# Optimization experiments

Hardware: AMD Instinct MI355X
Metric: run time of the kernel (lower is better)

## Reference

```python
import jax, jax.numpy as jnp
import numpy as np

HEADS = 1
EPS = 1e-12  # torch F.normalize eps


def dwt_haar(x):
    # Haar analysis, J=1, zero mode (even H,W -> no padding needed).
    b, c, H, W = x.shape
    xr = x.reshape(b, c, H // 2, 2, W // 2, 2)
    a = xr[:, :, :, 0, :, 0]
    bb = xr[:, :, :, 0, :, 1]
    cc = xr[:, :, :, 1, :, 0]
    d = xr[:, :, :, 1, :, 1]
    ll = (a + bb + cc + d) * 0.5
    h1 = (a - bb + cc - d) * 0.5  # high in width
    h2 = (a + bb - cc - d) * 0.5  # high in height
    h3 = (a - bb - cc + d) * 0.5  # diagonal
    return ll, h1, h2, h3


def idwt_haar(ll, h1, h2, h3):
    a = (ll + h1 + h2 + h3) * 0.5
    bb = (ll - h1 + h2 - h3) * 0.5
    cc = (ll + h1 - h2 - h3) * 0.5
    d = (ll - h1 - h2 + h3) * 0.5
    row0 = jnp.stack([a, bb], axis=-1)   # (b,c,h2,w2,2)
    row1 = jnp.stack([cc, d], axis=-1)
    y = jnp.stack([row0, row1], axis=3)  # (b,c,h2,2,w2,2)
    b_, c_, h2_, _, w2_, _ = y.shape
    return y.reshape(b_, c_, h2_ * 2, w2_ * 2)


def conv1x1(x, w, bias):
    # x: (b,c,h,w); w: (o,c); bias: (o,)
    return jnp.einsum('oc,bchw->bohw', w, x) + bias[None, :, None, None]


def mdta(x, qw, qb, kw, kb, vw, vb, pw, pb, temp):
    b, c, h, w = x.shape
    q = conv1x1(x, qw, qb).reshape(b, HEADS, c // HEADS, h * w)
    k = conv1x1(x, kw, kb).reshape(b, HEADS, c // HEADS, h * w)
    v = conv1x1(x, vw, vb).reshape(b, HEADS, c // HEADS, h * w)
    q = q / jnp.maximum(jnp.linalg.norm(q, axis=-1, keepdims=True), EPS)
    k = k / jnp.maximum(jnp.linalg.norm(k, axis=-1, keepdims=True), EPS)
    attn = jnp.einsum('bhcn,bhdn->bhcd', q, k) * temp[None]
    attn = jax.nn.softmax(attn, axis=-1)
    out = jnp.einsum('bhcd,bhdn->bhcn', attn, v).reshape(b, c, h, w)
    return conv1x1(out, pw, pb)


def setup_inputs() -> dict:
    key = jax.random.key(0)
    ks = jax.random.split(key, 20)
    B, C, H, W = 16, 64, 256, 256
    C3 = 3 * C
    s1 = 1.0 / np.sqrt(C)
    s3 = 1.0 / np.sqrt(C3)
    d = {'img': jax.random.normal(ks[0], (B, C, H, W), jnp.float32)}
    names = ['qw', 'qb', 'kw', 'kb', 'vw', 'vb', 'pw', 'pb']
    for i, n in enumerate(names):
        if n.endswith('w'):
            d['ll_' + n] = jax.random.normal(ks[1 + i], (C, C), jnp.float32) * s1
            d['h_' + n] = jax.random.normal(ks[10 + i], (C3, C3), jnp.float32) * s3
        else:
            d['ll_' + n] = jax.random.normal(ks[1 + i], (C,), jnp.float32) * s1
            d['h_' + n] = jax.random.normal(ks[10 + i], (C3,), jnp.float32) * s3
    d['ll_temp'] = jnp.ones((HEADS, 1, 1), jnp.float32)
    d['h_temp'] = jnp.ones((HEADS, 1, 1), jnp.float32)
    return d


def reference(img, ll_qw, ll_qb, ll_kw, ll_kb, ll_vw, ll_vb, ll_pw, ll_pb, ll_temp,
              h_qw, h_qb, h_kw, h_kb, h_vw, h_vb, h_pw, h_pb, h_temp):
    b, c, H, W = img.shape
    ll, h1, h2, h3 = dwt_haar(img)
    # rearrange 'b c fp h w -> b (c fp) h w' with fp=3 (bands interleaved per channel)
    hh = jnp.stack([h1, h2, h3], axis=2).reshape(b, c * 3, H // 2, W // 2)
    ll = mdta(ll, ll_qw, ll_qb, ll_kw, ll_kb, ll_vw, ll_vb, ll_pw, ll_pb, ll_temp)
    hh = mdta(hh, h_qw, h_qb, h_kw, h_kb, h_vw, h_vb, h_pw, h_pb, h_temp)
    hh = hh.reshape(b, c, 3, H // 2, W // 2)
    return idwt_haar(ll, hh[:, :, 0], hh[:, :, 1], hh[:, :, 2])
```

## Files before the change

### kernel.cpp

```cpp
#include <hip/hip_runtime.h>

typedef __bf16 bf16;
typedef bf16 bf16x8 __attribute__((ext_vector_type(8)));
typedef bf16 bf16x4 __attribute__((ext_vector_type(4)));
typedef float f32x4 __attribute__((ext_vector_type(4)));

#define NB 16
#define CLL 64
#define CHH 192
#define NPIX 16384

__global__ __launch_bounds__(256) void k_dwt(const float* __restrict__ img, bf16* __restrict__ xll,
                      bf16* __restrict__ xhh, float* __restrict__ sll, float* __restrict__ shh) {
    int bc = blockIdx.y;
    int b = bc >> 6, c = bc & 63;
    int t = threadIdx.x;
    int r = blockIdx.x * 16 + (t >> 4);
    int q = t & 15;
    const float* p0 = img + ((size_t)bc << 16) + (size_t)(2 * r) * 256 + 16 * q;
    const float* p1 = p0 + 256;
    float4 e0[4], e1[4];
    #pragma unroll
    for (int l = 0; l < 4; l++) { e0[l] = ((const float4*)p0)[l]; e1[l] = ((const float4*)p1)[l]; }
    const float* f0 = (const float*)e0;
    const float* f1 = (const float*)e1;
    bf16x8 vll, v1, v2, v3;
    float s0 = 0.f, s1 = 0.f, s2 = 0.f, s3 = 0.f;
    #pragma unroll
    for (int p = 0; p < 8; p++) {
        float a = f0[2 * p], bb = f0[2 * p + 1], cc = f1[2 * p], d = f1[2 * p + 1];
        float wll = (a + bb + cc + d) * 0.5f;
        float w1  = (a - bb + cc - d) * 0.5f;
        float w2  = (a + bb - cc - d) * 0.5f;
        float w3  = (a - bb - cc + d) * 0.5f;
        vll[p] = (bf16)wll; v1[p] = (bf16)w1; v2[p] = (bf16)w2; v3[p] = (bf16)w3;
        s0 += wll; s1 += w1; s2 += w2; s3 += w3;
    }
    size_t n = (size_t)r * 128 + 8 * q;
    *(bf16x8*)(xll + ((size_t)b * CLL + c) * NPIX + n) = vll;
    size_t hb = ((size_t)b * CHH + 3 * c) * NPIX + n;
    *(bf16x8*)(xhh + hb) = v1;
    *(bf16x8*)(xhh + hb + NPIX) = v2;
    *(bf16x8*)(xhh + hb + 2 * NPIX) = v3;
    for (int o = 32; o; o >>= 1) {
        s0 += __shfl_down(s0, o); s1 += __shfl_down(s1, o);
        s2 += __shfl_down(s2, o); s3 += __shfl_down(s3, o);
    }
    if ((t & 63) == 0) {
        atomicAdd(&sll[b * CLL + c], s0);
        atomicAdd(&shh[b * CHH + 3 * c + 0], s1);
        atomicAdd(&shh[b * CHH + 3 * c + 1], s2);
        atomicAdd(&shh[b * CHH + 3 * c + 2], s3);
    }
}

template <int C, int SPLITK>
__global__ __launch_bounds__(256) void k_gram(const bf16* __restrict__ X, float* __restrict__ G) {
    constexpr int T = C / 64;
    constexpr int NT = T * (T + 1) / 2;
    constexpr int KC = NPIX / SPLITK;
    __shared__ bf16 sA[64 * 64];
    __shared__ bf16 sB[64 * 64];
    int id = blockIdx.x;
    int sk = id % SPLITK; id /= SPLITK;
    int tl = id % NT;     id /= NT;
    int b = id;
    int ti = 0, tt = tl;
    while (tt >= T - ti) { tt -= T - ti; ti++; }
    int tj = ti + tt;
    const bf16* Xb = X + (size_t)b * C * NPIX;
    int t = threadIdx.x;
    int lane = t & 63, wv = t >> 6;
    int g = lane >> 4, l15 = lane & 15;

    int rowi = t >> 3, chunk = t & 7;
    int k0 = sk * KC;
    const bf16* gA0 = Xb + (size_t)(ti * 64 + rowi) * NPIX + k0 + chunk * 8;
    const bf16* gA1 = gA0 + (size_t)32 * NPIX;
    const bf16* gB0 = Xb + (size_t)(tj * 64 + rowi) * NPIX + k0 + chunk * 8;
    const bf16* gB1 = gB0 + (size_t)32 * NPIX;
    int swc = (chunk ^ (rowi & 7)) * 8;
    bf16* lA0 = sA + rowi * 64 + swc;
    bf16* lA1 = sA + (rowi + 32) * 64 + swc;
    bf16* lB0 = sB + rowi * 64 + swc;
    bf16* lB1 = sB + (rowi + 32) * 64 + swc;

    int arow = (wv >> 1) * 32;
    int bcol = (wv & 1) * 32;
    int sw = l15 & 7;
    int roA0 = (arow + l15) * 64, roA1 = roA0 + 16 * 64;
    int roB0 = (bcol + l15) * 64, roB1 = roB0 + 16 * 64;

    f32x4 acc[2][2] = {};
    bf16x8 rA0 = *(const bf16x8*)gA0;
    bf16x8 rA1 = *(const bf16x8*)gA1;
    bf16x8 rB0 = *(const bf16x8*)gB0;
    bf16x8 rB1 = *(const bf16x8*)gB1;
    for (int kc = 0; kc < KC; kc += 64) {
        *(bf16x8*)lA0 = rA0; *(bf16x8*)lA1 = rA1;
        *(bf16x8*)lB0 = rB0; *(bf16x8*)lB1 = rB1;
        __syncthreads();
        if (kc + 64 < KC) {
            rA0 = *(const bf16x8*)(gA0 + kc + 64);
            rA1 = *(const bf16x8*)(gA1 + kc + 64);
            rB0 = *(const bf16x8*)(gB0 + kc + 64);
            rB1 = *(const bf16x8*)(gB1 + kc + 64);
        }
        #pragma unroll
        for (int ks = 0; ks < 2; ks++) {
            int ck = ((ks * 4 + g) ^ sw) * 8;
            bf16x8 a0 = *(const bf16x8*)(sA + roA0 + ck);
            bf16x8 a1 = *(const bf16x8*)(sA + roA1 + ck);
            bf16x8 b0 = *(const bf16x8*)(sB + roB0 + ck);
            bf16x8 b1 = *(const bf16x8*)(sB + roB1 + ck);
            acc[0][0] = __builtin_amdgcn_mfma_f32_16x16x32_bf16(a0, b0, acc[0][0], 0, 0, 0);
            acc[0][1] = __builtin_amdgcn_mfma_f32_16x16x32_bf16(a0, b1, acc[0][1], 0, 0, 0);
            acc[1][0] = __builtin_amdgcn_mfma_f32_16x16x32_bf16(a1, b0, acc[1][0], 0, 0, 0);
            acc[1][1] = __builtin_amdgcn_mfma_f32_16x16x32_bf16(a1, b1, acc[1][1], 0, 0, 0);
        }
        __syncthreads();
    }
    float* Gb = G + (size_t)b * C * C;
    int r0q = ti * 64 + arow;
    int c0q = tj * 64 + bcol;
    #pragma unroll
    for (int rr = 0; rr < 2; rr++)
        #pragma unroll
        for (int c2 = 0; c2 < 2; c2++)
            #pragma unroll
            for (int rg = 0; rg < 4; rg++) {
                int row = r0q + rr * 16 + g * 4 + rg;
                int col = c0q + c2 * 16 + l15;
                atomicAdd(&Gb[(size_t)row * C + col], acc[rr][c2][rg]);
            }
}

__global__ void k_prep(float* __restrict__ Gll, float* __restrict__ Ghh,
                       const float* __restrict__ llvw, const float* __restrict__ hvw,
                       float* __restrict__ vwTll, float* __restrict__ vwThh) {
    const int S1 = CLL * CLL, S2 = CLL * CLL + CHH * CHH;
    int b = blockIdx.y;
    int idx = blockIdx.x * 256 + threadIdx.x;
    if (idx < S1) {
        float* Gb = Gll + (size_t)b * S1;
        int i = idx / CLL, j = idx % CLL;
        if (j < i) Gb[idx] = Gb[(size_t)j * CLL + i];
    } else if (idx < S2) {
        int id2 = idx - S1;
        float* Gb = Ghh + (size_t)b * (CHH * CHH);
        int i = id2 / CHH, j = id2 % CHH;
        if (j < i) Gb[id2] = Gb[(size_t)j * CHH + i];
    } else if (b == 0) {
        int k2 = idx - S2;
        if (k2 < S1) {
            int r = k2 / CLL, k = k2 % CLL;
            vwTll[k2] = llvw[(size_t)k * CLL + r];
        } else {
            int k3 = k2 - S1;
            if (k3 < CHH * CHH) {
                int r = k3 / CHH, k = k3 % CHH;
                vwThh[k3] = hvw[(size_t)k * CHH + r];
            }
        }
    }
}

template <typename OUT>
__global__ __launch_bounds__(256) void k_ntu(
        const float* __restrict__ Xll0, const float* __restrict__ Xll1, long XllbS,
        const float* __restrict__ Yll, long YllbS,
        OUT* __restrict__ Oll, long OllzS, long OllbS,
        const float* __restrict__ Xhh0, const float* __restrict__ Xhh1, long XhhbS,
        const float* __restrict__ Yhh, long YhhbS,
        OUT* __restrict__ Ohh, long OhhzS, long OhhbS) {
    int x = blockIdx.x, b = blockIdx.y, z = blockIdx.z;
    int C, rt, ct;
    const float *X, *Y;
    OUT* O;
    if (x == 0) {
        C = CLL; rt = 0; ct = 0;
        X = (z ? Xll1 : Xll0) + (size_t)b * XllbS;
        Y = Yll + (size_t)b * YllbS;
        O = Oll + (size_t)z * OllzS + (size_t)b * OllbS;
    } else {
        C = CHH; int tl = x - 1; rt = tl / 3; ct = tl % 3;
        X = (z ? Xhh1 : Xhh0) + (size_t)b * XhhbS;
        Y = Yhh + (size_t)b * YhhbS;
        O = Ohh + (size_t)z * OhhzS + (size_t)b * OhhbS;
    }
    int t = threadIdx.x, ti = t >> 4, tj = t & 15;
    const float* xr = X + (size_t)(rt * 64 + ti * 4) * C;
    const float* yr = Y + (size_t)(ct * 64 + tj * 4) * C;
    float acc[4][4] = {};
    for (int k = 0; k < C; k += 4) {
        float4 xa[4], yb[4];
        #pragma unroll
        for (int a = 0; a < 4; a++) xa[a] = *(const float4*)(xr + (size_t)a * C + k);
        #pragma unroll
        for (int q = 0; q < 4; q++) yb[q] = *(const float4*)(yr + (size_t)q * C + k);
        #pragma unroll
        for (int a = 0; a < 4; a++)
            #pragma unroll
            for (int q = 0; q < 4; q++)
                acc[a][q] += xa[a].x * yb[q].x + xa[a].y * yb[q].y
                           + xa[a].z * yb[q].z + xa[a].w * yb[q].w;
    }
    #pragma unroll
    for (int a = 0; a < 4; a++) {
        int row = rt * 64 + ti * 4 + a, col = ct * 64 + tj * 4;
        if constexpr (sizeof(OUT) == 4) {
            *(float4*)((float*)O + (size_t)row * C + col) =
                make_float4(acc[a][0], acc[a][1], acc[a][2], acc[a][3]);
        } else {
            bf16x4 v;
            v[0] = (bf16)acc[a][0]; v[1] = (bf16)acc[a][1];
            v[2] = (bf16)acc[a][2]; v[3] = (bf16)acc[a][3];
            *(bf16x4*)((bf16*)O + (size_t)row * C + col) = v;
        }
    }
}

__global__ __launch_bounds__(256) void k_nrm(const float* __restrict__ PRll,
        const float* __restrict__ PRhh,
        const float* __restrict__ llqw, const float* __restrict__ llkw,
        const float* __restrict__ hqw,  const float* __restrict__ hkw,
        const float* __restrict__ llqb, const float* __restrict__ llkb,
        const float* __restrict__ hqb,  const float* __restrict__ hkb,
        const float* __restrict__ sll,  const float* __restrict__ shh,
        float* __restrict__ nrmll, float* __restrict__ nrmhh,
        float* __restrict__ wsll,  float* __restrict__ wshh) {
    int z = blockIdx.z, b = blockIdx.y;
    int wv = threadIdx.x >> 6, lane = threadIdx.x & 63;
    int gr = blockIdx.x * 4 + wv;
    int C, i; const float *P, *w, *wb, *s; float *nrm, *ws;
    if (gr < CLL) {
        C = CLL; i = gr;
        P = PRll + ((size_t)z * NB + b) * CLL * CLL;
        w = z ? llkw : llqw; wb = z ? llkb : llqb;
        s = sll + (size_t)b * CLL;
        nrm = nrmll + ((size_t)z * NB + b) * CLL;
        ws  = wsll  + ((size_t)z * NB + b) * CLL;
    } else {
        C = CHH; i = gr - CLL;
        P = PRhh + ((size_t)z * NB + b) * CHH * CHH;
        w = z ? hkw : hqw; wb = z ? hkb : hqb;
        s = shh + (size_t)b * CHH;
        nrm = nrmhh + ((size_t)z * NB + b) * CHH;
        ws  = wshh  + ((size_t)z * NB + b) * CHH;
    }
    const float* Pi = P + (size_t)i * C;
    const float* wi = w + (size_t)i * C;
    float np = 0.f, sd = 0.f;
    for (int j = lane; j < C; j += 64) {
        float wj = wi[j];
        np += Pi[j] * wj;
        sd += wj * s[j];
    }
    for (int o = 32; o; o >>= 1) { np += __shfl_down(np, o); sd += __shfl_down(sd, o); }
    if (lane == 0) {
        float wbi = wb[i];
        float q2 = np + 2.f * wbi * sd + (float)NPIX * wbi * wbi;
        nrm[i] = fmaxf(sqrtf(fmaxf(q2, 0.f)), 1e-12f);
        ws[i] = sd;
    }
}

__global__ __launch_bounds__(256) void k_soft2(
        const float* __restrict__ Lll, const float* __restrict__ Lhh,
        const float* __restrict__ llkb, const float* __restrict__ llqb,
        const float* __restrict__ hkb,  const float* __restrict__ hqb,
        const float* __restrict__ nrmll, const float* __restrict__ nrmhh,
        const float* __restrict__ wsll,  const float* __restrict__ wshh,
        const float* __restrict__ llvb,  const float* __restrict__ hvb,
        const float* __restrict__ lltp,  const float* __restrict__ htp,
        float* __restrict__ All, float* __restrict__ Ahh,
        float* __restrict__ avll, float* __restrict__ avhh) {
    int b = blockIdx.y;
    int wv = threadIdx.x >> 6, lane = threadIdx.x & 63;
    int gr = blockIdx.x * 4 + wv;
    int C, i; const float *Lb, *kb, *qb, *qn, *kn, *qs, *ks, *vb, *tp;
    float *A, *av;
    if (gr < CLL) {
        C = CLL; i = gr;
        Lb = Lll + (size_t)b * CLL * CLL; kb = llkb; qb = llqb;
        qn = nrmll + (size_t)b * CLL;  kn = nrmll + ((size_t)NB + b) * CLL;
        qs = wsll + (size_t)b * CLL;   ks = wsll + ((size_t)NB + b) * CLL;
        vb = llvb; tp = lltp;
        A = All + (size_t)b * CLL * CLL; av = avll + (size_t)b * CLL;
    } else {
        C = CHH; i = gr - CLL;
        Lb = Lhh + (size_t)b * CHH * CHH; kb = hkb; qb = hqb;
        qn = nrmhh + (size_t)b * CHH;  kn = nrmhh + ((size_t)NB + b) * CHH;
        qs = wshh + (size_t)b * CHH;   ks = wshh + ((size_t)NB + b) * CHH;
        vb = hvb; tp = htp;
        A = Ahh + (size_t)b * CHH * CHH; av = avhh + (size_t)b * CHH;
    }
    const float* Li = Lb + (size_t)i * C;
    float qni = qn[i], qsi = qs[i], qbi = qb[i], tmp = tp[0];
    float Lv[3];
    #pragma unroll
    for (int s2 = 0; s2 < 3; s2++) {
        int j = lane + s2 * 64;
        if (j < C) {
            float l = Li[j] + qsi * kb[j] + qbi * ks[j] + (float)NPIX * qbi * kb[j];
            Lv[s2] = l / (qni * kn[j]) * tmp;
        } else Lv[s2] = -1e30f;
    }
    float mx = fmaxf(fmaxf(Lv[0], Lv[1]), Lv[2]);
    for (int o = 32; o; o >>= 1) mx = fmaxf(mx, __shfl_xor(mx, o));
    float e[3], sum = 0.f;
    #pragma unroll
    for (int s2 = 0; s2 < 3; s2++) {
        e[s2] = (lane + s2 * 64 < C) ? expf(Lv[s2] - mx) : 0.f;
        sum += e[s2];
    }
    for (int o = 32; o; o >>= 1) sum += __shfl_xor(sum, o);
    float inv = 1.f / sum;
    float avp = 0.f;
    #pragma unroll
    for (int s2 = 0; s2 < 3; s2++) {
        int j = lane + s2 * 64;
        if (j < C) {
            float a = e[s2] * inv;
            A[(size_t)i * C + j] = a;
            avp += a * vb[j];
        }
    }
    for (int o = 32; o; o >>= 1) avp += __shfl_down(avp, o);
    if (lane == 0) av[i] = avp;
}

__global__ __launch_bounds__(256) void k_mv(const float* __restrict__ llpw,
        const float* __restrict__ llpb, const float* __restrict__ hpw,
        const float* __restrict__ hpb, const float* __restrict__ avll,
        const float* __restrict__ avhh, float* __restrict__ mvll, float* __restrict__ mvhh) {
    int b = blockIdx.y;
    int wv = threadIdx.x >> 6, lane = threadIdx.x & 63;
    int gr = blockIdx.x * 4 + wv;
    int C, i; const float *pw, *pb_, *av_; float* mv_;
    if (gr < CLL) {
        C = CLL; i = gr;
        pw = llpw; pb_ = llpb; av_ = avll + (size_t)b * CLL; mv_ = mvll + (size_t)b * CLL;
    } else {
        C = CHH; i = gr - CLL;
        pw = hpw; pb_ = hpb; av_ = avhh + (size_t)b * CHH; mv_ = mvhh + (size_t)b * CHH;
    }
    const float* pwi = pw + (size_t)i * C;
    float m = 0.f;
    for (int k = lane; k < C; k += 64) m += pwi[k] * av_[k];
    for (int o = 32; o; o >>= 1) m += __shfl_down(m, o);
    if (lane == 0) mv_[i] = m + pb_[i];
}

__global__ __launch_bounds__(256) void k_final(const bf16* __restrict__ xll, const bf16* __restrict__ xhh,
                        const bf16* __restrict__ Mll, const bf16* __restrict__ Mhh,
                        const float* __restrict__ mvll, const float* __restrict__ mvhh,
                        float* __restrict__ out) {
    __shared__ alignas(16) float smemf[256 * 65];
    bf16* sxl = (bf16*)smemf;
    bf16* sxh = (bf16*)smemf + 64 * 64;
    float* Y = smemf;
    int b = blockIdx.y, tile = blockIdx.x;
    int irow = tile >> 1, j0 = (tile & 1) << 6;
    int n0 = irow * 128 + j0;
    int t = threadIdx.x;
    const bf16* Xl = xll + (size_t)b * CLL * NPIX;
    const bf16* Xh = xhh + (size_t)b * CHH * NPIX;
    for (int task = t; task < 512; task += 256) {
        int d = task >> 3, q = task & 7;
        bf16x8 v = *(const bf16x8*)(Xl + (size_t)d * NPIX + n0 + q * 8);
        int cs = (((d >> 3) ^ q) << 3) | (d & 7);
        #pragma unroll
        for (int p = 0; p < 8; p++) sxl[(q * 8 + p) * 64 + cs] = v[p];
    }
    for (int task = t; task < 1536; task += 256) {
        int d = task >> 3, q = task & 7;
        bf16x8 v = *(const bf16x8*)(Xh + (size_t)d * NPIX + n0 + q * 8);
        int c = d >> 3;
        int cs = ((((c & ~7) | ((c & 7) ^ q))) << 3) | (d & 7);
        #pragma unroll
        for (int p = 0; p < 8; p++) sxh[(q * 8 + p) * 192 + cs] = v[p];
    }
    __syncthreads();
    int wv = t >> 6, lane = t & 63, g = lane >> 4, l15 = lane & 15;
    f32x4 accL[4] = {};
    {
        const bf16* M = Mll + (size_t)b * CLL * CLL + (size_t)(wv * 16 + l15) * CLL;
        #pragma unroll
        for (int ks = 0; ks < 2; ks++) {
            bf16x8 af = *(const bf16x8*)(M + ks * 32 + g * 8);
            int cc = ks * 4 + g;
            #pragma unroll
            for (int c2 = 0; c2 < 4; c2++) {
                int pxr = c2 * 16 + l15;
                int csw = cc ^ ((pxr >> 3) & 7);
                bf16x8 bfrag = *(const bf16x8*)(sxl + pxr * 64 + csw * 8);
                accL[c2] = __builtin_amdgcn_mfma_f32_16x16x32_bf16(af, bfrag, accL[c2], 0, 0, 0);
            }
        }
    }
    f32x4 accH[3][4] = {};
    {
        const bf16* M = Mhh + (size_t)b * CHH * CHH;
        #pragma unroll 2
        for (int kb = 0; kb < CHH; kb += 32) {
            bf16x8 af[3];
            #pragma unroll
            for (int r = 0; r < 3; r++)
                af[r] = *(const bf16x8*)(M + (size_t)(wv * 48 + r * 16 + l15) * CHH + kb + g * 8);
            #pragma unroll
            for (int c2 = 0; c2 < 4; c2++) {
                int pxr = c2 * 16 + l15;
                int cc = (kb >> 3) + g;
                int csw = (cc & ~7) | ((cc & 7) ^ ((pxr >> 3) & 7));
                bf16x8 bfrag = *(const bf16x8*)(sxh + pxr * 192 + csw * 8);
                #pragma unroll
                for (int r = 0; r < 3; r++)
                    accH[r][c2] = __builtin_amdgcn_mfma_f32_16x16x32_bf16(af[r], bfrag, accH[r][c2], 0, 0, 0);
            }
        }
    }
    __syncthreads();
    #pragma unroll
    for (int c2 = 0; c2 < 4; c2++)
        #pragma unroll
        for (int rg = 0; rg < 4; rg++) {
            int rl = wv * 16 + g * 4 + rg;
            Y[rl * 65 + c2 * 16 + l15] = accL[c2][rg] + mvll[b * CLL + rl];
        }
    #pragma unroll
    for (int r = 0; r < 3; r++)
        #pragma unroll
        for (int c2 = 0; c2 < 4; c2++)
            #pragma unroll
            for (int rg = 0; rg < 4; rg++) {
                int rh = wv * 48 + r * 16 + g * 4 + rg;
                Y[(64 + rh) * 65 + c2 * 16 + l15] = accH[r][c2][rg] + mvhh[b * CHH + rh];
            }
    __syncthreads();
    int p = t & 63, cg = t >> 6;
    float* ob = out + ((size_t)b * CLL) * 65536;
    for (int it = 0; it < 16; it++) {
        int c = it * 4 + cg;
        float ll = Y[c * 65 + p];
        float h1 = Y[(64 + 3 * c + 0) * 65 + p];
        float h2 = Y[(64 + 3 * c + 1) * 65 + p];
        float h3 = Y[(64 + 3 * c + 2) * 65 + p];
        float a  = (ll + h1 + h2 + h3) * 0.5f;
        float bb = (ll - h1 + h2 - h3) * 0.5f;
        float cc = (ll + h1 - h2 - h3) * 0.5f;
        float d  = (ll - h1 - h2 + h3) * 0.5f;
        int jj = j0 + p;
        float2* o0 = (float2*)(ob + ((size_t)c * 256 + 2 * irow) * 256 + 2 * jj);
        float2* o1 = (float2*)(ob + ((size_t)c * 256 + 2 * irow + 1) * 256 + 2 * jj);
        *o0 = make_float2(a, bb);
        *o1 = make_float2(cc, d);
    }
}

extern "C" void kernel_launch(void* const* d_in, const int* in_sizes, int n_in,
                              void* d_out, int out_size, void* d_ws, size_t ws_size,
                              hipStream_t stream) {
    const float* img    = (const float*)d_in[0];
    const float* ll_qw = (const float*)d_in[1];  const float* h_qw = (const float*)d_in[2];
    const float* ll_qb = (const float*)d_in[3];  const float* h_qb = (const float*)d_in[4];
    const float* ll_kw = (const float*)d_in[5];  const float* h_kw = (const float*)d_in[6];
    const float* ll_kb = (const float*)d_in[7];  const float* h_kb = (const float*)d_in[8];
    const float* ll_vw = (const float*)d_in[9];  const float* h_vw = (const float*)d_in[10];
    const float* ll_vb = (const float*)d_in[11]; const float* h_vb = (const float*)d_in[12];
    const float* ll_pw = (const float*)d_in[13]; const float* h_pw = (const float*)d_in[14];
    const float* ll_pb = (const float*)d_in[15]; const float* h_pb = (const float*)d_in[16];
    const float* ll_tp = (const float*)d_in[17]; const float* h_tp = (const float*)d_in[18];
    float* out = (float*)d_out;

    char* ws = (char*)d_ws;
    size_t off = 0;
    auto alloc = [&](size_t sz) { char* p = ws + off; off += (sz + 255) & ~(size_t)255; return p; };
    const size_t SL = (size_t)CLL * CLL, SH = (size_t)CHH * CHH;
    bf16*  xll  = (bf16*) alloc((size_t)NB * CLL * NPIX * 2);
    bf16*  xhh  = (bf16*) alloc((size_t)NB * CHH * NPIX * 2);
    char*  zb   = ws + off;
    float* sll  = (float*)alloc(NB * CLL * 4);
    float* shh  = (float*)alloc(NB * CHH * 4);
    float* Gll  = (float*)alloc(NB * SL * 4);
    float* Ghh  = (float*)alloc(NB * SH * 4);
    size_t zsz  = (size_t)((ws + off) - zb);
    float* PRll = (float*)alloc(2 * NB * SL * 4);
    float* PRhh = (float*)alloc(2 * NB * SH * 4);
    float* nrmll= (float*)alloc(2 * NB * CLL * 4);
    float* nrmhh= (float*)alloc(2 * NB * CHH * 4);
    float* wsll = (float*)alloc(2 * NB * CLL * 4);
    float* wshh = (float*)alloc(2 * NB * CHH * 4);
    float* Lll  = (float*)alloc(NB * SL * 4);
    float* Lhh  = (float*)alloc(NB * SH * 4);
    float* All  = (float*)alloc(NB * SL * 4);
    float* Ahh  = (float*)alloc(NB * SH * 4);
    float* avll = (float*)alloc(NB * CLL * 4);   float* avhh = (float*)alloc(NB * CHH * 4);
    float* WTll = (float*)alloc(NB * SL * 4);
    float* WThh = (float*)alloc(NB * SH * 4);
    float* vwTll= (float*)alloc(SL * 4);
    float* vwThh= (float*)alloc(SH * 4);
    bf16*  Mll  = (bf16*) alloc(NB * SL * 2);
    bf16*  Mhh  = (bf16*) alloc(NB * SH * 2);
    float* mvll = (float*)alloc(NB * CLL * 4);   float* mvhh = (float*)alloc(NB * CHH * 4);

    hipMemsetAsync(zb, 0, zsz, stream);

    k_dwt<<<dim3(8, NB * 64), 256, 0, stream>>>(img, xll, xhh, sll, shh);

    k_gram<CLL, 16><<<NB * 1 * 16, 256, 0, stream>>>(xll, Gll);
    k_gram<CHH, 8><<<NB * 6 * 8, 256, 0, stream>>>(xhh, Ghh);

    k_prep<<<dim3((2 * (int)(SL + SH) + 255) / 256, NB), 256, 0, stream>>>(
        Gll, Ghh, ll_vw, h_vw, vwTll, vwThh);

    k_ntu<float><<<dim3(10, NB, 2), 256, 0, stream>>>(
        ll_qw, ll_kw, 0, Gll, (long)SL, PRll, (long)(NB * SL), (long)SL,
        h_qw,  h_kw,  0, Ghh, (long)SH, PRhh, (long)(NB * SH), (long)SH);

    k_nrm<<<dim3(64, NB, 2), 256, 0, stream>>>(PRll, PRhh,
        ll_qw, ll_kw, h_qw, h_kw, ll_qb, ll_kb, h_qb, h_kb, sll, shh,
        nrmll, nrmhh, wsll, wshh);

    k_ntu<float><<<dim3(10, NB, 1), 256, 0, stream>>>(
        PRll, PRll, (long)SL, ll_kw, 0, Lll, 0, (long)SL,
        PRhh, PRhh, (long)SH, h_kw,  0, Lhh, 0, (long)SH);

    k_soft2<<<dim3(64, NB), 256, 0, stream>>>(Lll, Lhh, ll_kb, ll_qb, h_kb, h_qb,
        nrmll, nrmhh, wsll, wshh, ll_vb, h_vb, ll_tp, h_tp, All, Ahh, avll, avhh);

    k_mv<<<dim3(64, NB), 256, 0, stream>>>(ll_pw, ll_pb, h_pw, h_pb, avll, avhh, mvll, mvhh);

    k_ntu<float><<<dim3(10, NB, 1), 256, 0, stream>>>(
        vwTll, vwTll, 0, All, (long)SL, WTll, 0, (long)SL,
        vwThh, vwThh, 0, Ahh, (long)SH, WThh, 0, (long)SH);

    k_ntu<bf16><<<dim3(10, NB, 1), 256, 0, stream>>>(
        ll_pw, ll_pw, 0, WTll, (long)SL, Mll, 0, (long)SL,
        h_pw,  h_pw,  0, WThh, (long)SH, Mhh, 0, (long)SH);

    k_final<<<dim3(256, NB), 256, 0, stream>>>(xll, xhh, Mll, Mhh, mvll, mvhh, out);
}
```

Baseline: 441.5 us.

## Fuse pipeline stages into persistent kernels with device-wide barriers

Merges the DWT and Gram computation into one persistent kernel and the nine small middle kernels (symmetrize, projections, norms, softmax, matvec, weight products) into a second persistent kernel. Stages are separated by atomic-counter grid barriers instead of separate launches. The aim is to cut launch overhead and inter-kernel gaps for the many tiny stages. The risks are deadlock if the 1024 or 320 blocks are not all co-resident, and the spin-wait cost; the DWT also now does 8 row-groups per block.

```diff
diff --git a/kernel.cpp b/kernel.cpp
--- a/kernel.cpp
+++ b/kernel.cpp
@@ -10,87 +10,99 @@
 #define CHH 192
 #define NPIX 16384
 
-__global__ __launch_bounds__(256) void k_dwt(const float* __restrict__ img, bf16* __restrict__ xll,
-                      bf16* __restrict__ xhh, float* __restrict__ sll, float* __restrict__ shh) {
-    int bc = blockIdx.y;
-    int b = bc >> 6, c = bc & 63;
-    int t = threadIdx.x;
-    int r = blockIdx.x * 16 + (t >> 4);
-    int q = t & 15;
-    const float* p0 = img + ((size_t)bc << 16) + (size_t)(2 * r) * 256 + 16 * q;
-    const float* p1 = p0 + 256;
-    float4 e0[4], e1[4];
-    #pragma unroll
-    for (int l = 0; l < 4; l++) { e0[l] = ((const float4*)p0)[l]; e1[l] = ((const float4*)p1)[l]; }
-    const float* f0 = (const float*)e0;
-    const float* f1 = (const float*)e1;
-    bf16x8 vll, v1, v2, v3;
-    float s0 = 0.f, s1 = 0.f, s2 = 0.f, s3 = 0.f;
-    #pragma unroll
-    for (int p = 0; p < 8; p++) {
-        float a = f0[2 * p], bb = f0[2 * p + 1], cc = f1[2 * p], d = f1[2 * p + 1];
-        float wll = (a + bb + cc + d) * 0.5f;
-        float w1  = (a - bb + cc - d) * 0.5f;
-        float w2  = (a + bb - cc - d) * 0.5f;
-        float w3  = (a - bb - cc + d) * 0.5f;
-        vll[p] = (bf16)wll; v1[p] = (bf16)w1; v2[p] = (bf16)w2; v3[p] = (bf16)w3;
-        s0 += wll; s1 += w1; s2 += w2; s3 += w3;
-    }
-    size_t n = (size_t)r * 128 + 8 * q;
-    *(bf16x8*)(xll + ((size_t)b * CLL + c) * NPIX + n) = vll;
-    size_t hb = ((size_t)b * CHH + 3 * c) * NPIX + n;
-    *(bf16x8*)(xhh + hb) = v1;
-    *(bf16x8*)(xhh + hb + NPIX) = v2;
-    *(bf16x8*)(xhh + hb + 2 * NPIX) = v3;
-    for (int o = 32; o; o >>= 1) {
-        s0 += __shfl_down(s0, o); s1 += __shfl_down(s1, o);
-        s2 += __shfl_down(s2, o); s3 += __shfl_down(s3, o);
-    }
-    if ((t & 63) == 0) {
-        atomicAdd(&sll[b * CLL + c], s0);
-        atomicAdd(&shh[b * CHH + 3 * c + 0], s1);
-        atomicAdd(&shh[b * CHH + 3 * c + 1], s2);
-        atomicAdd(&shh[b * CHH + 3 * c + 2], s3);
-    }
+__device__ __forceinline__ void dev_barrier(unsigned* ctr, int id, unsigned target) {
+    __syncthreads();
+    __threadfence();
+    if (threadIdx.x == 0) {
+        __hip_atomic_fetch_add(&ctr[id], 1u, __ATOMIC_RELEASE, __HIP_MEMORY_SCOPE_AGENT);
+        while (__hip_atomic_load(&ctr[id], __ATOMIC_ACQUIRE, __HIP_MEMORY_SCOPE_AGENT) < target)
+            __builtin_amdgcn_s_sleep(2);
+        __threadfence();
+    }
+    __syncthreads();
 }
 
-template <int C, int SPLITK>
-__global__ __launch_bounds__(256) void k_gram(const bf16* __restrict__ X, float* __restrict__ G) {
-    constexpr int T = C / 64;
-    constexpr int NT = T * (T + 1) / 2;
-    constexpr int KC = NPIX / SPLITK;
+__global__ __launch_bounds__(256, 4) void k_front(const float* __restrict__ img,
+        bf16* __restrict__ xll, bf16* __restrict__ xhh,
+        float* __restrict__ sll, float* __restrict__ shh,
+        float* __restrict__ Gll, float* __restrict__ Ghh, unsigned* __restrict__ ctr) {
     __shared__ bf16 sA[64 * 64];
     __shared__ bf16 sB[64 * 64];
-    int id = blockIdx.x;
-    int sk = id % SPLITK; id /= SPLITK;
-    int tl = id % NT;     id /= NT;
-    int b = id;
-    int ti = 0, tt = tl;
-    while (tt >= T - ti) { tt -= T - ti; ti++; }
-    int tj = ti + tt;
-    const bf16* Xb = X + (size_t)b * C * NPIX;
-    int t = threadIdx.x;
+    int blk = blockIdx.x, t = threadIdx.x;
+    {
+        int bc = blk;
+        int b = bc >> 6, c = bc & 63;
+        int q = t & 15;
+        float s0 = 0.f, s1 = 0.f, s2 = 0.f, s3 = 0.f;
+        for (int it = 0; it < 8; it++) {
+            int r = it * 16 + (t >> 4);
+            const float* p0 = img + ((size_t)bc << 16) + (size_t)(2 * r) * 256 + 16 * q;
+            const float* p1 = p0 + 256;
+            float4 e0[4], e1[4];
+            #pragma unroll
+            for (int l = 0; l < 4; l++) { e0[l] = ((const float4*)p0)[l]; e1[l] = ((const float4*)p1)[l]; }
+            const float* f0 = (const float*)e0;
+            const float* f1 = (const float*)e1;
+            bf16x8 vll, v1, v2, v3;
+            #pragma unroll
+            for (int p = 0; p < 8; p++) {
+                float a = f0[2 * p], bb = f0[2 * p + 1], cc = f1[2 * p], d = f1[2 * p + 1];
+                float wll = (a + bb + cc + d) * 0.5f;
+                float w1  = (a - bb + cc - d) * 0.5f;
+                float w2  = (a + bb - cc - d) * 0.5f;
+                float w3  = (a - bb - cc + d) * 0.5f;
+                vll[p] = (bf16)wll; v1[p] = (bf16)w1; v2[p] = (bf16)w2; v3[p] = (bf16)w3;
+                s0 += wll; s1 += w1; s2 += w2; s3 += w3;
+            }
+            size_t n = (size_t)r * 128 + 8 * q;
+            *(bf16x8*)(xll + ((size_t)b * CLL + c) * NPIX + n) = vll;
+            size_t hb = ((size_t)b * CHH + 3 * c) * NPIX + n;
+            *(bf16x8*)(xhh + hb) = v1;
+            *(bf16x8*)(xhh + hb + NPIX) = v2;
+            *(bf16x8*)(xhh + hb + 2 * NPIX) = v3;
+        }
+        for (int o = 32; o; o >>= 1) {
+            s0 += __shfl_down(s0, o); s1 += __shfl_down(s1, o);
+            s2 += __shfl_down(s2, o); s3 += __shfl_down(s3, o);
+        }
+        if ((t & 63) == 0) {
+            atomicAdd(&sll[b * CLL + c], s0);
+            atomicAdd(&shh[b * CHH + 3 * c + 0], s1);
+            atomicAdd(&shh[b * CHH + 3 * c + 1], s2);
+            atomicAdd(&shh[b * CHH + 3 * c + 2], s3);
+        }
+    }
+    dev_barrier(ctr, 0, gridDim.x);
+    int C, ti, tj, sk, b2, KC;
+    const bf16* X; float* G;
+    if (blk < 768) {
+        C = CHH; sk = blk % 8; int tl = (blk / 8) % 6; b2 = blk / 48; KC = 2048;
+        ti = (tl < 3) ? 0 : ((tl < 5) ? 1 : 2);
+        tj = (tl < 3) ? tl : ((tl < 5) ? tl - 2 : 2);
+        X = xhh + (size_t)b2 * CHH * NPIX; G = Ghh + (size_t)b2 * CHH * CHH;
+    } else {
+        int j = blk - 768;
+        C = CLL; sk = j % 16; b2 = j / 16; KC = 1024; ti = 0; tj = 0;
+        X = xll + (size_t)b2 * CLL * NPIX; G = Gll + (size_t)b2 * CLL * CLL;
+    }
     int lane = t & 63, wv = t >> 6;
     int g = lane >> 4, l15 = lane & 15;
-
     int rowi = t >> 3, chunk = t & 7;
     int k0 = sk * KC;
-    const bf16* gA0 = Xb + (size_t)(ti * 64 + rowi) * NPIX + k0 + chunk * 8;
+    const bf16* gA0 = X + (size_t)(ti * 64 + rowi) * NPIX + k0 + chunk * 8;
     const bf16* gA1 = gA0 + (size_t)32 * NPIX;
-    const bf16* gB0 = Xb + (size_t)(tj * 64 + rowi) * NPIX + k0 + chunk * 8;
+    const bf16* gB0 = X + (size_t)(tj * 64 + rowi) * NPIX + k0 + chunk * 8;
     const bf16* gB1 = gB0 + (size_t)32 * NPIX;
     int swc = (chunk ^ (rowi & 7)) * 8;
     bf16* lA0 = sA + rowi * 64 + swc;
     bf16* lA1 = sA + (rowi + 32) * 64 + swc;
     bf16* lB0 = sB + rowi * 64 + swc;
     bf16* lB1 = sB + (rowi + 32) * 64 + swc;
-
     int arow = (wv >> 1) * 32;
     int bcol = (wv & 1) * 32;
     int sw = l15 & 7;
     int roA0 = (arow + l15) * 64, roA1 = roA0 + 16 * 64;
     int roB0 = (bcol + l15) * 64, roB1 = roB0 + 16 * 64;
-
     f32x4 acc[2][2] = {};
     bf16x8 rA0 = *(const bf16x8*)gA0;
     bf16x8 rA1 = *(const bf16x8*)gA1;
@@ -120,7 +132,6 @@
         }
         __syncthreads();
     }
-    float* Gb = G + (size_t)b * C * C;
     int r0q = ti * 64 + arow;
     int c0q = tj * 64 + bcol;
     #pragma unroll
@@ -131,62 +142,28 @@
             for (int rg = 0; rg < 4; rg++) {
                 int row = r0q + rr * 16 + g * 4 + rg;
                 int col = c0q + c2 * 16 + l15;
-                atomicAdd(&Gb[(size_t)row * C + col], acc[rr][c2][rg]);
+                atomicAdd(&G[(size_t)row * C + col], acc[rr][c2][rg]);
             }
 }
 
-__global__ void k_prep(float* __restrict__ Gll, float* __restrict__ Ghh,
-                       const float* __restrict__ llvw, const float* __restrict__ hvw,
-                       float* __restrict__ vwTll, float* __restrict__ vwThh) {
-    const int S1 = CLL * CLL, S2 = CLL * CLL + CHH * CHH;
-    int b = blockIdx.y;
-    int idx = blockIdx.x * 256 + threadIdx.x;
-    if (idx < S1) {
-        float* Gb = Gll + (size_t)b * S1;
-        int i = idx / CLL, j = idx % CLL;
-        if (j < i) Gb[idx] = Gb[(size_t)j * CLL + i];
-    } else if (idx < S2) {
-        int id2 = idx - S1;
-        float* Gb = Ghh + (size_t)b * (CHH * CHH);
-        int i = id2 / CHH, j = id2 % CHH;
-        if (j < i) Gb[id2] = Gb[(size_t)j * CHH + i];
-    } else if (b == 0) {
-        int k2 = idx - S2;
-        if (k2 < S1) {
-            int r = k2 / CLL, k = k2 % CLL;
-            vwTll[k2] = llvw[(size_t)k * CLL + r];
-        } else {
-            int k3 = k2 - S1;
-            if (k3 < CHH * CHH) {
-                int r = k3 / CHH, k = k3 % CHH;
-                vwThh[k3] = hvw[(size_t)k * CHH + r];
-            }
-        }
-    }
-}
-
-template <typename OUT>
-__global__ __launch_bounds__(256) void k_ntu(
-        const float* __restrict__ Xll0, const float* __restrict__ Xll1, long XllbS,
-        const float* __restrict__ Yll, long YllbS,
-        OUT* __restrict__ Oll, long OllzS, long OllbS,
-        const float* __restrict__ Xhh0, const float* __restrict__ Xhh1, long XhhbS,
-        const float* __restrict__ Yhh, long YhhbS,
-        OUT* __restrict__ Ohh, long OhhzS, long OhhbS) {
-    int x = blockIdx.x, b = blockIdx.y, z = blockIdx.z;
+__device__ __forceinline__ void ntu_body(int x, int b, int z,
+        const float* Xll0, const float* Xll1, long XllbS, const float* Yll, long YllbS,
+        void* Oll, long OllzS, long OllbS,
+        const float* Xhh0, const float* Xhh1, long XhhbS, const float* Yhh, long YhhbS,
+        void* Ohh, long OhhzS, long OhhbS, bool obf16) {
     int C, rt, ct;
     const float *X, *Y;
-    OUT* O;
+    char* O; long OzS, ObS;
     if (x == 0) {
         C = CLL; rt = 0; ct = 0;
         X = (z ? Xll1 : Xll0) + (size_t)b * XllbS;
         Y = Yll + (size_t)b * YllbS;
-        O = Oll + (size_t)z * OllzS + (size_t)b * OllbS;
+        O = (char*)Oll; OzS = OllzS; ObS = OllbS;
     } else {
         C = CHH; int tl = x - 1; rt = tl / 3; ct = tl % 3;
         X = (z ? Xhh1 : Xhh0) + (size_t)b * XhhbS;
         Y = Yhh + (size_t)b * YhhbS;
-        O = Ohh + (size_t)z * OhhzS + (size_t)b * OhhbS;
+        O = (char*)Ohh; OzS = OhhzS; ObS = OhhbS;
     }
     int t = threadIdx.x, ti = t >> 4, tj = t & 15;
     const float* xr = X + (size_t)(rt * 64 + ti * 4) * C;
@@ -208,148 +185,195 @@
     #pragma unroll
     for (int a = 0; a < 4; a++) {
         int row = rt * 64 + ti * 4 + a, col = ct * 64 + tj * 4;
-        if constexpr (sizeof(OUT) == 4) {
-            *(float4*)((float*)O + (size_t)row * C + col) =
+        if (!obf16) {
+            float* Op = (float*)O + (size_t)z * OzS + (size_t)b * ObS;
+            *(float4*)(Op + (size_t)row * C + col) =
                 make_float4(acc[a][0], acc[a][1], acc[a][2], acc[a][3]);
         } else {
+            bf16* Op = (bf16*)O + (size_t)z * OzS + (size_t)b * ObS;
             bf16x4 v;
             v[0] = (bf16)acc[a][0]; v[1] = (bf16)acc[a][1];
             v[2] = (bf16)acc[a][2]; v[3] = (bf16)acc[a][3];
-            *(bf16x4*)((bf16*)O + (size_t)row * C + col) = v;
+            *(bf16x4*)(Op + (size_t)row * C + col) = v;
         }
     }
 }
 
-__global__ __launch_bounds__(256) void k_nrm(const float* __restrict__ PRll,
-        const float* __restrict__ PRhh,
-        const float* __restrict__ llqw, const float* __restrict__ llkw,
-        const float* __restrict__ hqw,  const float* __restrict__ hkw,
-        const float* __restrict__ llqb, const float* __restrict__ llkb,
-        const float* __restrict__ hqb,  const float* __restrict__ hkb,
-        const float* __restrict__ sll,  const float* __restrict__ shh,
-        float* __restrict__ nrmll, float* __restrict__ nrmhh,
-        float* __restrict__ wsll,  float* __restrict__ wshh) {
-    int z = blockIdx.z, b = blockIdx.y;
-    int wv = threadIdx.x >> 6, lane = threadIdx.x & 63;
-    int gr = blockIdx.x * 4 + wv;
-    int C, i; const float *P, *w, *wb, *s; float *nrm, *ws;
-    if (gr < CLL) {
-        C = CLL; i = gr;
-        P = PRll + ((size_t)z * NB + b) * CLL * CLL;
-        w = z ? llkw : llqw; wb = z ? llkb : llqb;
-        s = sll + (size_t)b * CLL;
-        nrm = nrmll + ((size_t)z * NB + b) * CLL;
-        ws  = wsll  + ((size_t)z * NB + b) * CLL;
+__global__ __launch_bounds__(256, 2) void k_mid(
+        float* __restrict__ Gll, float* __restrict__ Ghh,
+        const float* llqw, const float* llqb, const float* llkw, const float* llkb,
+        const float* llvw, const float* llvb, const float* llpw, const float* llpb,
+        const float* hqw, const float* hqb, const float* hkw, const float* hkb,
+        const float* hvw, const float* hvb, const float* hpw, const float* hpb,
+        const float* lltp, const float* htp,
+        const float* sll, const float* shh,
+        float* PRll, float* PRhh, float* nrmll, float* nrmhh, float* wsll, float* wshh,
+        float* Lll, float* Lhh, float* All, float* Ahh, float* avll, float* avhh,
+        float* WTll, float* WThh, float* vwTll, float* vwThh,
+        bf16* Mll, bf16* Mhh, float* mvll, float* mvhh, unsigned* ctr) {
+    const long SL = (long)CLL * CLL, SH = (long)CHH * CHH;
+    int blk = blockIdx.x, t = threadIdx.x;
+    int nb = gridDim.x;
+    int wv = t >> 6, lane = t & 63;
+    {
+        const int S1 = CLL * CLL, S2 = CHH * CHH;
+        int total = NB * (S1 + S2) + (S1 + S2);
+        for (int idx = blk * 256 + t; idx < total; idx += nb * 256) {
+            if (idx < NB * (S1 + S2)) {
+                int b = idx / (S1 + S2); int r = idx % (S1 + S2);
+                if (r < S1) {
+                    float* Gb = Gll + (size_t)b * S1;
+                    int i = r / CLL, j = r % CLL;
+                    if (j < i) Gb[r] = Gb[(size_t)j * CLL + i];
+                } else {
+                    int r2 = r - S1;
+                    float* Gb = Ghh + (size_t)b * S2;
+                    int i = r2 / CHH, j = r2 % CHH;
+                    if (j < i) Gb[r2] = Gb[(size_t)j * CHH + i];
+                }
+            } else {
+                int r = idx - NB * (S1 + S2);
+                if (r < S1) {
+                    int rr = r / CLL, k = r % CLL;
+                    vwTll[r] = llvw[(size_t)k * CLL + rr];
+                } else {
+                    int r2 = r - S1;
+                    int rr = r2 / CHH, k = r2 % CHH;
+                    vwThh[r2] = hvw[(size_t)k * CHH + rr];
+                }
+            }
+        }
+    }
+    dev_barrier(ctr, 1, nb);
+    {
+        int x = blk % 10, b = (blk / 10) % 16, z = blk / 160;
+        ntu_body(x, b, z, llqw, llkw, 0, Gll, SL, PRll, (long)NB * SL, SL,
+                 hqw, hkw, 0, Ghh, SH, PRhh, (long)NB * SH, SH, false);
+    }
+    dev_barrier(ctr, 2, nb);
+    for (int wt = blk * 4 + wv; wt < 8192; wt += nb * 4) {
+        int z = wt >> 12, b = (wt >> 8) & 15, gr = wt & 255;
+        int C, i; const float *P, *w, *wb, *s; float *nrm, *ws;
+        if (gr < CLL) {
+            C = CLL; i = gr;
+            P = PRll + ((size_t)z * NB + b) * SL;
+            w = z ? llkw : llqw; wb = z ? llkb : llqb;
+            s = sll + (size_t)b * CLL;
+            nrm = nrmll + ((size_t)z * NB + b) * CLL;
+            ws  = wsll  + ((size_t)z * NB + b) * CLL;
+        } else {
+            C = CHH; i = gr - CLL;
+            P = PRhh + ((size_t)z * NB + b) * SH;
+            w = z ? hkw : hqw; wb = z ? hkb : hqb;
+            s = shh + (size_t)b * CHH;
+            nrm = nrmhh + ((size_t)z * NB + b) * CHH;
+            ws  = wshh  + ((size_t)z * NB + b) * CHH;
+        }
+        const float* Pi = P + (size_t)i * C;
+        const float* wi = w + (size_t)i * C;
+        float np = 0.f, sd = 0.f;
+        for (int j = lane; j < C; j += 64) {
+            float wj = wi[j];
+            np += Pi[j] * wj;
+            sd += wj * s[j];
+        }
+        for (int o = 32; o; o >>= 1) { np += __shfl_down(np, o); sd += __shfl_down(sd, o); }
+        if (lane == 0) {
+            float wbi = wb[i];
+            float q2 = np + 2.f * wbi * sd + (float)NPIX * wbi * wbi;
+            nrm[i] = fmaxf(sqrtf(fmaxf(q2, 0.f)), 1e-12f);
+            ws[i] = sd;
+        }
+    }
+    dev_barrier(ctr, 3, nb);
+    if (blk < 160) {
+        int x = blk % 10, b = blk / 10;
+        ntu_body(x, b, 0, PRll, PRll, SL, llkw, 0, Lll, 0, SL,
+                 PRhh, PRhh, SH, hkw, 0, Lhh, 0, SH, false);
+    }
+    dev_barrier(ctr, 4, nb);
+    for (int wt = blk * 4 + wv; wt < 4096; wt += nb * 4) {
+        int b = wt >> 8, gr = wt & 255;
+        int C, i; const float *Lb, *kb, *qb, *qn, *kn, *qs, *ks, *vb, *tp;
+        float *A, *av;
+        if (gr < CLL) {
+            C = CLL; i = gr;
+            Lb = Lll + (size_t)b * SL; kb = llkb; qb = llqb;
+            qn = nrmll + (size_t)b * CLL;  kn = nrmll + ((size_t)NB + b) * CLL;
+            qs = wsll + (size_t)b * CLL;   ks = wsll + ((size_t)NB + b) * CLL;
+            vb = llvb; tp = lltp;
+            A = All + (size_t)b * SL; av = avll + (size_t)b * CLL;
+        } else {
+            C = CHH; i = gr - CLL;
+            Lb = Lhh + (size_t)b * SH; kb = hkb; qb = hqb;
+            qn = nrmhh + (size_t)b * CHH;  kn = nrmhh + ((size_t)NB + b) * CHH;
+            qs = wshh + (size_t)b * CHH;   ks = wshh + ((size_t)NB + b) * CHH;
+            vb = hvb; tp = htp;
+            A = Ahh + (size_t)b * SH; av = avhh + (size_t)b * CHH;
+        }
+        const float* Li = Lb + (size_t)i * C;
+        float qni = qn[i], qsi = qs[i], qbi = qb[i], tmp = tp[0];
+        float Lv[3];
+        #pragma unroll
+        for (int s2 = 0; s2 < 3; s2++) {
+            int j = lane + s2 * 64;
+            if (j < C) {
+                float l = Li[j] + qsi * kb[j] + qbi * ks[j] + (float)NPIX * qbi * kb[j];
+                Lv[s2] = l / (qni * kn[j]) * tmp;
+            } else Lv[s2] = -1e30f;
+        }
+        float mx = fmaxf(fmaxf(Lv[0], Lv[1]), Lv[2]);
+        for (int o = 32; o; o >>= 1) mx = fmaxf(mx, __shfl_xor(mx, o));
+        float e[3], sum = 0.f;
+        #pragma unroll
+        for (int s2 = 0; s2 < 3; s2++) {
+            e[s2] = (lane + s2 * 64 < C) ? expf(Lv[s2] - mx) : 0.f;
+            sum += e[s2];
+        }
+        for (int o = 32; o; o >>= 1) sum += __shfl_xor(sum, o);
+        float inv = 1.f / sum;
+        float avp = 0.f;
+        #pragma unroll
+        for (int s2 = 0; s2 < 3; s2++) {
+            int j = lane + s2 * 64;
+            if (j < C) {
+                float a = e[s2] * inv;
+                A[(size_t)i * C + j] = a;
+                avp += a * vb[j];
+            }
+        }
+        for (int o = 32; o; o >>= 1) avp += __shfl_down(avp, o);
+        if (lane == 0) av[i] = avp;
+    }
+    dev_barrier(ctr, 5, nb);
+    if (blk >= 160) {
+        for (int wt = (blk - 160) * 4 + wv; wt < 4096; wt += 160 * 4) {
+            int b = wt >> 8, gr = wt & 255;
+            int C, i; const float *pw, *pb_, *av_; float* mv_;
+            if (gr < CLL) {
+                C = CLL; i = gr;
+                pw = llpw; pb_ = llpb; av_ = avll + (size_t)b * CLL; mv_ = mvll + (size_t)b * CLL;
+            } else {
+                C = CHH; i = gr - CLL;
+                pw = hpw; pb_ = hpb; av_ = avhh + (size_t)b * CHH; mv_ = mvhh + (size_t)b * CHH;
+            }
+            const float* pwi = pw + (size_t)i * C;
+            float m = 0.f;
+            for (int k = lane; k < C; k += 64) m += pwi[k] * av_[k];
+            for (int o = 32; o; o >>= 1) m += __shfl_down(m, o);
+            if (lane == 0) mv_[i] = m + pb_[i];
+        }
     } else {
-        C = CHH; i = gr - CLL;
-        P = PRhh + ((size_t)z * NB + b) * CHH * CHH;
-        w = z ? hkw : hqw; wb = z ? hkb : hqb;
-        s = shh + (size_t)b * CHH;
-        nrm = nrmhh + ((size_t)z * NB + b) * CHH;
-        ws  = wshh  + ((size_t)z * NB + b) * CHH;
-    }
-    const float* Pi = P + (size_t)i * C;
-    const float* wi = w + (size_t)i * C;
-    float np = 0.f, sd = 0.f;
-    for (int j = lane; j < C; j += 64) {
-        float wj = wi[j];
-        np += Pi[j] * wj;
-        sd += wj * s[j];
-    }
-    for (int o = 32; o; o >>= 1) { np += __shfl_down(np, o); sd += __shfl_down(sd, o); }
-    if (lane == 0) {
-        float wbi = wb[i];
-        float q2 = np + 2.f * wbi * sd + (float)NPIX * wbi * wbi;
-        nrm[i] = fmaxf(sqrtf(fmaxf(q2, 0.f)), 1e-12f);
-        ws[i] = sd;
-    }
-}
-
-__global__ __launch_bounds__(256) void k_soft2(
-        const float* __restrict__ Lll, const float* __restrict__ Lhh,
-        const float* __restrict__ llkb, const float* __restrict__ llqb,
-        const float* __restrict__ hkb,  const float* __restrict__ hqb,
-        const float* __restrict__ nrmll, const float* __restrict__ nrmhh,
-        const float* __restrict__ wsll,  const float* __restrict__ wshh,
-        const float* __restrict__ llvb,  const float* __restrict__ hvb,
-        const float* __restrict__ lltp,  const float* __restrict__ htp,
-        float* __restrict__ All, float* __restrict__ Ahh,
-        float* __restrict__ avll, float* __restrict__ avhh) {
-    int b = blockIdx.y;
-    int wv = threadIdx.x >> 6, lane = threadIdx.x & 63;
-    int gr = blockIdx.x * 4 + wv;
-    int C, i; const float *Lb, *kb, *qb, *qn, *kn, *qs, *ks, *vb, *tp;
-    float *A, *av;
-    if (gr < CLL) {
-        C = CLL; i = gr;
-        Lb = Lll + (size_t)b * CLL * CLL; kb = llkb; qb = llqb;
-        qn = nrmll + (size_t)b * CLL;  kn = nrmll + ((size_t)NB + b) * CLL;
-        qs = wsll + (size_t)b * CLL;   ks = wsll + ((size_t)NB + b) * CLL;
-        vb = llvb; tp = lltp;
-        A = All + (size_t)b * CLL * CLL; av = avll + (size_t)b * CLL;
-    } else {
-        C = CHH; i = gr - CLL;
-        Lb = Lhh + (size_t)b * CHH * CHH; kb = hkb; qb = hqb;
-        qn = nrmhh + (size_t)b * CHH;  kn = nrmhh + ((size_t)NB + b) * CHH;
-        qs = wshh + (size_t)b * CHH;   ks = wshh + ((size_t)NB + b) * CHH;
-        vb = hvb; tp = htp;
-        A = Ahh + (size_t)b * CHH * CHH; av = avhh + (size_t)b * CHH;
-    }
-    const float* Li = Lb + (size_t)i * C;
-    float qni = qn[i], qsi = qs[i], qbi = qb[i], tmp = tp[0];
-    float Lv[3];
-    #pragma unroll
-    for (int s2 = 0; s2 < 3; s2++) {
-        int j = lane + s2 * 64;
-        if (j < C) {
-            float l = Li[j] + qsi * kb[j] + qbi * ks[j] + (float)NPIX * qbi * kb[j];
-            Lv[s2] = l / (qni * kn[j]) * tmp;
-        } else Lv[s2] = -1e30f;
-    }
-    float mx = fmaxf(fmaxf(Lv[0], Lv[1]), Lv[2]);
-    for (int o = 32; o; o >>= 1) mx = fmaxf(mx, __shfl_xor(mx, o));
-    float e[3], sum = 0.f;
-    #pragma unroll
-    for (int s2 = 0; s2 < 3; s2++) {
-        e[s2] = (lane + s2 * 64 < C) ? expf(Lv[s2] - mx) : 0.f;
-        sum += e[s2];
-    }
-    for (int o = 32; o; o >>= 1) sum += __shfl_xor(sum, o);
-    float inv = 1.f / sum;
-    float avp = 0.f;
-    #pragma unroll
-    for (int s2 = 0; s2 < 3; s2++) {
-        int j = lane + s2 * 64;
-        if (j < C) {
-            float a = e[s2] * inv;
-            A[(size_t)i * C + j] = a;
-            avp += a * vb[j];
-        }
-    }
-    for (int o = 32; o; o >>= 1) avp += __shfl_down(avp, o);
-    if (lane == 0) av[i] = avp;
-}
-
-__global__ __launch_bounds__(256) void k_mv(const float* __restrict__ llpw,
-        const float* __restrict__ llpb, const float* __restrict__ hpw,
-        const float* __restrict__ hpb, const float* __restrict__ avll,
-        const float* __restrict__ avhh, float* __restrict__ mvll, float* __restrict__ mvhh) {
-    int b = blockIdx.y;
-    int wv = threadIdx.x >> 6, lane = threadIdx.x & 63;
-    int gr = blockIdx.x * 4 + wv;
-    int C, i; const float *pw, *pb_, *av_; float* mv_;
-    if (gr < CLL) {
-        C = CLL; i = gr;
-        pw = llpw; pb_ = llpb; av_ = avll + (size_t)b * CLL; mv_ = mvll + (size_t)b * CLL;
-    } else {
-        C = CHH; i = gr - CLL;
-        pw = hpw; pb_ = hpb; av_ = avhh + (size_t)b * CHH; mv_ = mvhh + (size_t)b * CHH;
-    }
-    const float* pwi = pw + (size_t)i * C;
-    float m = 0.f;
-    for (int k = lane; k < C; k += 64) m += pwi[k] * av_[k];
-    for (int o = 32; o; o >>= 1) m += __shfl_down(m, o);
-    if (lane == 0) mv_[i] = m + pb_[i];
+        int x = blk % 10, b = blk / 10;
+        ntu_body(x, b, 0, vwTll, vwTll, 0, All, SL, WTll, 0, SL,
+                 vwThh, vwThh, 0, Ahh, SH, WThh, 0, SH, false);
+    }
+    dev_barrier(ctr, 6, nb);
+    if (blk < 160) {
+        int x = blk % 10, b = blk / 10;
+        ntu_body(x, b, 0, llpw, llpw, 0, WTll, SL, Mll, 0, SL,
+                 hpw, hpw, 0, WThh, SH, Mhh, 0, SH, true);
+    }
 }
 
 __global__ __launch_bounds__(256) void k_final(const bf16* __restrict__ xll, const bf16* __restrict__ xhh,
@@ -482,6 +506,7 @@
     char*  zb   = ws + off;
     float* sll  = (float*)alloc(NB * CLL * 4);
     float* shh  = (float*)alloc(NB * CHH * 4);
+    unsigned* ctr = (unsigned*)alloc(64 * 4);
     float* Gll  = (float*)alloc(NB * SL * 4);
     float* Ghh  = (float*)alloc(NB * SH * 4);
     size_t zsz  = (size_t)((ws + off) - zb);
@@ -506,38 +531,15 @@
 
     hipMemsetAsync(zb, 0, zsz, stream);
 
-    k_dwt<<<dim3(8, NB * 64), 256, 0, stream>>>(img, xll, xhh, sll, shh);
-
-    k_gram<CLL, 16><<<NB * 1 * 16, 256, 0, stream>>>(xll, Gll);
-    k_gram<CHH, 8><<<NB * 6 * 8, 256, 0, stream>>>(xhh, Ghh);
-
-    k_prep<<<dim3((2 * (int)(SL + SH) + 255) / 256, NB), 256, 0, stream>>>(
-        Gll, Ghh, ll_vw, h_vw, vwTll, vwThh);
-
-    k_ntu<float><<<dim3(10, NB, 2), 256, 0, stream>>>(
-        ll_qw, ll_kw, 0, Gll, (long)SL, PRll, (long)(NB * SL), (long)SL,
-        h_qw,  h_kw,  0, Ghh, (long)SH, PRhh, (long)(NB * SH), (long)SH);
-
-    k_nrm<<<dim3(64, NB, 2), 256, 0, stream>>>(PRll, PRhh,
-        ll_qw, ll_kw, h_qw, h_kw, ll_qb, ll_kb, h_qb, h_kb, sll, shh,
-        nrmll, nrmhh, wsll, wshh);
-
-    k_ntu<float><<<dim3(10, NB, 1), 256, 0, stream>>>(
-        PRll, PRll, (long)SL, ll_kw, 0, Lll, 0, (long)SL,
-        PRhh, PRhh, (long)SH, h_kw,  0, Lhh, 0, (long)SH);
-
-    k_soft2<<<dim3(64, NB), 256, 0, stream>>>(Lll, Lhh, ll_kb, ll_qb, h_kb, h_qb,
-        nrmll, nrmhh, wsll, wshh, ll_vb, h_vb, ll_tp, h_tp, All, Ahh, avll, avhh);
-
-    k_mv<<<dim3(64, NB), 256, 0, stream>>>(ll_pw, ll_pb, h_pw, h_pb, avll, avhh, mvll, mvhh);
-
-    k_ntu<float><<<dim3(10, NB, 1), 256, 0, stream>>>(
-        vwTll, vwTll, 0, All, (long)SL, WTll, 0, (long)SL,
-        vwThh, vwThh, 0, Ahh, (long)SH, WThh, 0, (long)SH);
-
-    k_ntu<bf16><<<dim3(10, NB, 1), 256, 0, stream>>>(
-        ll_pw, ll_pw, 0, WTll, (long)SL, Mll, 0, (long)SL,
-        h_pw,  h_pw,  0, WThh, (long)SH, Mhh, 0, (long)SH);
+    k_front<<<1024, 256, 0, stream>>>(img, xll, xhh, sll, shh, Gll, Ghh, ctr);
+
+    k_mid<<<320, 256, 0, stream>>>(Gll, Ghh,
+        ll_qw, ll_qb, ll_kw, ll_kb, ll_vw, ll_vb, ll_pw, ll_pb,
+        h_qw, h_qb, h_kw, h_kb, h_vw, h_vb, h_pw, h_pb,
+        ll_tp, h_tp, sll, shh,
+        PRll, PRhh, nrmll, nrmhh, wsll, wshh,
+        Lll, Lhh, All, Ahh, avll, avhh,
+        WTll, WThh, vwTll, vwThh, Mll, Mhh, mvll, mvhh, ctr);
 
     k_final<<<dim3(256, NB), 256, 0, stream>>>(xll, xhh, Mll, Mhh, mvll, mvhh, out);
 }
```

Result: slower. 1.322 ms (+199.5%).
